# Kernel tuning notes

Hardware: AMD Instinct MI355X
Metric: run time of the kernel (lower is better)

The kernel has to match this reference:

```python
import jax, jax.numpy as jnp
import numpy as np

N, T, D = 2048, 32, 256
NE = T + 2                       # num_embeddings = 32 + 3 - 1
GK_MUL, GK_NUM = 2.0, 3
HEADS = (4, 1)

def _bn(x, g, b):
    # BatchNorm1d (training-mode batch stats, biased variance, eps=1e-5)
    m = x.mean(0)
    v = jnp.mean((x - m) ** 2, 0)
    return (x - m) * jax.lax.rsqrt(v + 1e-5) * g + b

def _gk(x):
    # multi-bandwidth Gaussian kernel over pairwise squared L2 distances
    sq = jnp.sum(x * x, -1)
    l2 = jnp.maximum(sq[:, None] + sq[None, :] - 2.0 * (x @ x.T), 0.0)
    n = x.shape[0]
    bw = jnp.sum(l2) / (n * n - n) / (GK_MUL ** (GK_NUM // 2))
    out = jnp.zeros_like(l2)
    for i in range(GK_NUM):
        out = out + jnp.exp(-l2 / (bw * (GK_MUL ** i)))
    return out

def _mlp3(x, w, b):
    h = jax.nn.relu(x @ w[0] + b[0])
    h = jax.nn.relu(h @ w[1] + b[1])
    return h @ w[2] + b[2]

def _ln(x, g, b):
    m = x.mean(-1, keepdims=True)
    v = jnp.mean((x - m) ** 2, -1, keepdims=True)
    return (x - m) * jax.lax.rsqrt(v + 1e-5) * g + b

def _posenc(t, d):
    pos = jnp.arange(t, dtype=jnp.float32)[:, None]
    div = jnp.exp(jnp.arange(0, d, 2, dtype=jnp.float32) * (-np.log(10000.0) / d))
    ang = pos * div
    return jnp.stack([jnp.sin(ang), jnp.cos(ang)], -1).reshape(t, d)

def _tlayer(x, mask, w, b, w1, b1, w2, b2, g, be, h):
    n, l, d = x.shape
    dh = d // h
    def split(t):
        return t.reshape(n, l, h, dh).transpose(0, 2, 1, 3)
    q = split(x @ w[0] + b[0])
    k = split(x @ w[1] + b[1])
    v = split(x @ w[2] + b[2])
    s = jnp.einsum('bhld,bhmd->bhlm', q, k) / np.sqrt(dh)
    s = jnp.where(mask[:, None, :, :], s, -1e9)
    o = jnp.einsum('bhlm,bhmd->bhld', jax.nn.softmax(s, -1), v)
    o = o.transpose(0, 2, 1, 3).reshape(n, l, d)
    x = _ln(x + o @ w[3] + b[3], g[0], be[0])
    f = jax.nn.relu(x @ w1 + b1) @ w2 + b2
    return _ln(x + f, g[1], be[1])

def _forward(emb0, emb1, emb2, simi_w, simi_b, bn_g, bn_b, simi_eps, dissim,
             gcn_w, gcn_b, adapt_w, adapt_b, type_emb, attn_w, attn_b,
             ffn_w1, ffn_b1, ffn_w2, ffn_b2, ln_g, ln_b,
             out_w1, out_b1, out_w2, out_b2, msk0, msk1, msk2):
    n = emb0.shape[0]
    embs = [emb0[:, 0, :], emb1, emb2]
    msks = [msk0[:, :1], msk1, msk2]               # [n,1] bool each
    mstk = jnp.stack(msks)                         # [3,n,1]
    mask_mats = mstk & jnp.swapaxes(mstk, 1, 2)    # [3,n,n]
    sim_sum = jnp.zeros((n, n), emb0.dtype)
    lstab = jnp.zeros((), emb0.dtype)
    for m in range(3):
        e = embs[m]
        p = _mlp3(e, simi_w[m], simi_b[m])
        wgk = _gk(_bn(jax.nn.relu(p), bn_g, bn_b))
        gk = _gk(_bn(e, bn_g, bn_b))
        eps = jax.nn.sigmoid(simi_eps[m])
        sim_sum = sim_sum + ((1.0 - eps) * wgk + eps) * gk * mask_mats[m]
        lstab = lstab + jnp.abs(jnp.linalg.norm(p) - jnp.linalg.norm(e))
    agg = sim_sum / mask_mats.sum(0).astype(emb0.dtype)
    agg = agg * (agg > jax.nn.sigmoid(dissim[0]))
    imputed = []
    for m in range(3):  # all modals are missing-capable
        h = jax.nn.relu(agg @ (embs[m] @ gcn_w[m, 0]) + gcn_b[m, 0])
        h = jax.nn.relu(agg @ (h @ gcn_w[m, 1]) + gcn_b[m, 1])
        s = jax.nn.sigmoid(embs[m] @ adapt_w[m].T + adapt_b[m])
        o = jax.nn.sigmoid(h @ adapt_w[m].T + adapt_b[m])  # adapt_self reused, bug kept from source
        s = s / (s + o)
        imp = s * embs[m] + (1.0 - s) * h
        mk = msks[m].astype(emb0.dtype)
        imputed.append(imp * mk + (1.0 - mk) * h)
    e0 = emb0.at[:, 0, :].set(imputed[0]) + type_emb[0]
    e0 = e0 + _posenc(emb0.shape[1], emb0.shape[2])
    e1 = imputed[1][:, None, :] + type_emb[1]
    e2 = imputed[2][:, None, :] + type_emb[2]
    z = jnp.concatenate([e0, e1, e2], 1)            # [n, NE, D]
    tok = jnp.concatenate([msk0, msk1, msk2], 1)    # [n, NE]
    amask = tok[:, :, None] & tok[:, None, :]       # [n, NE, NE]
    for li in range(2):
        z = jax.nn.relu(_tlayer(z, amask, attn_w[li], attn_b[li],
                                ffn_w1[li], ffn_b1[li], ffn_w2[li], ffn_b2[li],
                                ln_g[li], ln_b[li], HEADS[li]))
    comb = z.reshape(n, -1)
    y = jax.nn.relu(comb @ out_w1 + out_b1)
    y = (y @ out_w2 + out_b2).squeeze(-1)
    return y, lstab

def setup_inputs():
    key = jax.random.key(0)
    it = iter(jax.random.split(key, 32))
    def nrm(shape, s):
        return jax.random.normal(next(it), shape, jnp.float32) * s
    return {
        'emb0': nrm((N, T, D), 1.0),
        'emb1': nrm((N, D), 1.0),
        'emb2': nrm((N, D), 1.0),
        'msk0': jax.random.randint(next(it), (N, T), 0, 2).astype(bool),
        'msk1': jnp.ones((N, 1), bool),
        'msk2': jax.random.randint(next(it), (N, 1), 0, 2).astype(bool),
        'simi_w': nrm((3, 3, D, D), 0.06), 'simi_b': jnp.zeros((3, 3, D)),
        'bn_g': jnp.ones((D,)), 'bn_b': jnp.zeros((D,)),
        'simi_eps': jnp.ones((4,)), 'dissim': jnp.full((1,), 2.0),
        'gcn_w': nrm((3, 2, D, D), 0.06), 'gcn_b': jnp.zeros((3, 2, D)),
        'adapt_w': nrm((3, 1, D), 0.06), 'adapt_b': jnp.zeros((3, 1)),
        'type_emb': nrm((3, D), 0.02),
        'attn_w': nrm((2, 4, D, D), 0.06), 'attn_b': jnp.zeros((2, 4, D)),
        'ffn_w1': nrm((2, D, 4 * D), 0.06), 'ffn_b1': jnp.zeros((2, 4 * D)),
        'ffn_w2': nrm((2, 4 * D, D), 0.06), 'ffn_b2': jnp.zeros((2, D)),
        'ln_g': jnp.ones((2, 2, D)), 'ln_b': jnp.zeros((2, 2, D)),
        'out_w1': nrm((NE * D, 2 * D), 0.02), 'out_b1': jnp.zeros((2 * D,)),
        'out_w2': nrm((2 * D, 1), 0.02), 'out_b2': jnp.zeros((1,)),
    }

def reference(emb0, emb1, emb2, msk0, msk1, msk2, simi_w, simi_b, bn_g, bn_b,
              simi_eps, dissim, gcn_w, gcn_b, adapt_w, adapt_b, type_emb,
              attn_w, attn_b, ffn_w1, ffn_b1, ffn_w2, ffn_b2, ln_g, ln_b,
              out_w1, out_b1, out_w2, out_b2):
    return _forward(emb0, emb1, emb2, simi_w, simi_b, bn_g, bn_b, simi_eps,
                    dissim, gcn_w, gcn_b, adapt_w, adapt_b, type_emb, attn_w,
                    attn_b, ffn_w1, ffn_b1, ffn_w2, ffn_b2, ln_g, ln_b,
                    out_w1, out_b1, out_w2, out_b2, msk0, msk1, msk2)
```

## Files before the change

### kernel.cpp

```cpp
#include <hip/hip_runtime.h>
#include <hip/hip_bf16.h>


#define NN 2048
#define DD 256
#define LTOK 34

typedef __attribute__((ext_vector_type(8))) short bf16x8;
typedef __attribute__((ext_vector_type(4))) float f32x4;

__device__ __forceinline__ float bf2f(__hip_bfloat16 x) { return __bfloat162float(x); }
__device__ __forceinline__ __hip_bfloat16 f2bf(float x) { return __float2bfloat16(x); }
__device__ __forceinline__ float us2f(ushort u) {
    unsigned x = (unsigned)u << 16;
    float f;
    __builtin_memcpy(&f, &x, 4);
    return f;
}
__device__ __forceinline__ ushort f2us(float x) {
    __hip_bfloat16 h = f2bf(x);
    ushort u;
    __builtin_memcpy(&u, &h, 2);
    return u;
}

__device__ __forceinline__ float block_reduce_sum256(float v, float* red) {
    for (int o = 32; o > 0; o >>= 1) v += __shfl_down(v, o, 64);
    int tid = threadIdx.x;
    if ((tid & 63) == 0) red[tid >> 6] = v;
    __syncthreads();
    float s = red[0] + red[1] + red[2] + red[3];
    __syncthreads();
    return s;
}

__device__ __forceinline__ int xcd_remap(int lin, int nwg) {
    int q = nwg >> 3, r = nwg & 7;
    int xcd = lin & 7, pos = lin >> 3;
    return (xcd < r ? xcd * (q + 1) : r * (q + 1) + (xcd - r) * q) + pos;
}

__device__ __forceinline__ void stage_tile(const ushort* __restrict__ src,
                                           ushort* lds, int grow0, size_t ldk,
                                           int k0, int wv, int l) {
#pragma unroll
    for (int c = 0; c < 4; ++c) {
        int rowbase = wv * 32 + c * 8;
        int row = rowbase + (l >> 3);
        int sx = ((l & 7) ^ (row & 7)) * 8;
        __builtin_amdgcn_global_load_lds(
            (const __attribute__((address_space(1))) void*)(src + (size_t)(grow0 + row) * ldk + k0 + sx),
            (__attribute__((address_space(3))) void*)(lds + rowbase * 64), 16, 0, 0);
    }
}

__device__ __forceinline__ void stage_tile64(const ushort* __restrict__ src,
                                             ushort* lds, int grow0, size_t ldk,
                                             int k0, int wv, int l) {
#pragma unroll
    for (int c = 0; c < 2; ++c) {
        int rowbase = wv * 16 + c * 8;
        int row = rowbase + (l >> 3);
        int sx = ((l & 7) ^ (row & 7)) * 8;
        __builtin_amdgcn_global_load_lds(
            (const __attribute__((address_space(1))) void*)(src + (size_t)(grow0 + row) * ldk + k0 + sx),
            (__attribute__((address_space(3))) void*)(lds + rowbase * 64), 16, 0, 0);
    }
}

#define MFMA_STEP(ACC)                                                          \
    {                                                                           \
        bf16x8 av[4], bv[4];                                                    \
        _Pragma("unroll") for (int f = 0; f < 4; ++f) {                         \
            int ra = wr * 64 + f * 16 + lr;                                     \
            av[f] = *(const bf16x8*)(As + ra * 64 + (((kk * 4 + l16) ^ (ra & 7)) * 8)); \
            int rb = wc * 64 + f * 16 + lr;                                     \
            bv[f] = *(const bf16x8*)(Bs + rb * 64 + (((kk * 4 + l16) ^ (rb & 7)) * 8)); \
        }                                                                       \
        _Pragma("unroll") for (int mf = 0; mf < 4; ++mf)                        \
            _Pragma("unroll") for (int nf = 0; nf < 4; ++nf)                    \
                ACC[mf][nf] = __builtin_amdgcn_mfma_f32_16x16x32_bf16(          \
                    av[mf], bv[nf], ACC[mf][nf], 0, 0, 0);                      \
    }

template <int OUTM, bool BIAS, bool RELU>
__global__ __launch_bounds__(256) void gemm_mfma(
    const ushort* __restrict__ A, const ushort* __restrict__ Bt,
    const float* __restrict__ bias, void* __restrict__ Cout,
    int M, int N, int K, int ldt)
{
    __shared__ __align__(16) ushort As[128 * 64];
    __shared__ __align__(16) ushort Bs[128 * 64];
    const int gx = gridDim.x;
    int lin = xcd_remap(blockIdx.y * gx + blockIdx.x, gx * gridDim.y);
    const int bm = (lin / gx) * 128, bn = (lin % gx) * 128;
    const int tid = threadIdx.x;
    const int l = tid & 63, wv = tid >> 6;
    const int wr = wv >> 1, wc = wv & 1;
    const int l16 = l >> 4, lr = l & 15;
    const int kpz = K / gridDim.z;
    const int kbeg = blockIdx.z * kpz, kend = kbeg + kpz;
    f32x4 zero = {0.f, 0.f, 0.f, 0.f};
    f32x4 acc[4][4];
#pragma unroll
    for (int i = 0; i < 4; ++i)
#pragma unroll
        for (int j = 0; j < 4; ++j) acc[i][j] = zero;

    for (int k0 = kbeg; k0 < kend; k0 += 64) {
        stage_tile(A, As, bm, K, k0, wv, l);
        stage_tile(Bt, Bs, bn, K, k0, wv, l);
        __syncthreads();
#pragma unroll
        for (int kk = 0; kk < 2; ++kk) MFMA_STEP(acc)
        __syncthreads();
    }
    float* Cf = (float*)Cout + (size_t)blockIdx.z * M * N;
#pragma unroll
    for (int mf = 0; mf < 4; ++mf) {
#pragma unroll
        for (int nf = 0; nf < 4; ++nf) {
            int col = bn + wc * 64 + nf * 16 + lr;
            float bb = BIAS ? bias[col] : 0.f;
#pragma unroll
            for (int r = 0; r < 4; ++r) {
                int row = bm + wr * 64 + mf * 16 + l16 * 4 + r;
                float v = acc[mf][nf][r] + bb;
                if (OUTM == 3)
                    v += bf2f(((const __hip_bfloat16*)Cout)[(size_t)row * N + col]);
                if (RELU) v = fmaxf(v, 0.f);
                if (OUTM == 0)
                    Cf[(size_t)row * N + col] = v;
                else if (OUTM == 4) {
                    int r2 = row + 14 * (row / 34);
                    ((__hip_bfloat16*)Cout)[(size_t)col * ldt + r2] = f2bf(v);
                } else
                    ((__hip_bfloat16*)Cout)[(size_t)row * N + col] = f2bf(v);
            }
        }
    }
}

template <int OUTM, bool BIAS, bool RELU>
__global__ __launch_bounds__(256) void gemm_thin(
    const ushort* __restrict__ A, const ushort* __restrict__ Bt,
    const float* __restrict__ bias, void* __restrict__ Cout,
    int M, int N, int K)
{
    __shared__ __align__(16) ushort As[64 * 64];
    __shared__ __align__(16) ushort Bs[128 * 64];
    const int gx = gridDim.x;
    int lin = xcd_remap(blockIdx.y * gx + blockIdx.x, gx * gridDim.y);
    const int bm = (lin / gx) * 64, bn = (lin % gx) * 128;
    const int tid = threadIdx.x;
    const int l = tid & 63, wv = tid >> 6;
    const int wr = wv >> 1, wc = wv & 1;
    const int l16 = l >> 4, lr = l & 15;
    f32x4 zero = {0.f, 0.f, 0.f, 0.f};
    f32x4 acc[2][4];
#pragma unroll
    for (int i = 0; i < 2; ++i)
#pragma unroll
        for (int j = 0; j < 4; ++j) acc[i][j] = zero;

    for (int k0 = 0; k0 < K; k0 += 64) {
        stage_tile64(A, As, bm, K, k0, wv, l);
        stage_tile(Bt, Bs, bn, K, k0, wv, l);
        __syncthreads();
#pragma unroll
        for (int kk = 0; kk < 2; ++kk) {
            bf16x8 av[2], bv[4];
#pragma unroll
            for (int f = 0; f < 2; ++f) {
                int ra = wr * 32 + f * 16 + lr;
                av[f] = *(const bf16x8*)(As + ra * 64 + (((kk * 4 + l16) ^ (ra & 7)) * 8));
            }
#pragma unroll
            for (int f = 0; f < 4; ++f) {
                int rb = wc * 64 + f * 16 + lr;
                bv[f] = *(const bf16x8*)(Bs + rb * 64 + (((kk * 4 + l16) ^ (rb & 7)) * 8));
            }
#pragma unroll
            for (int mf = 0; mf < 2; ++mf)
#pragma unroll
                for (int nf = 0; nf < 4; ++nf)
                    acc[mf][nf] = __builtin_amdgcn_mfma_f32_16x16x32_bf16(
                        av[mf], bv[nf], acc[mf][nf], 0, 0, 0);
        }
        __syncthreads();
    }
#pragma unroll
    for (int mf = 0; mf < 2; ++mf) {
#pragma unroll
        for (int nf = 0; nf < 4; ++nf) {
            int col = bn + wc * 64 + nf * 16 + lr;
            float bb = BIAS ? bias[col] : 0.f;
#pragma unroll
            for (int r = 0; r < 4; ++r) {
                int row = bm + wr * 32 + mf * 16 + l16 * 4 + r;
                float v = acc[mf][nf][r] + bb;
                if (OUTM == 3)
                    v += bf2f(((const __hip_bfloat16*)Cout)[(size_t)row * N + col]);
                if (RELU) v = fmaxf(v, 0.f);
                ((__hip_bfloat16*)Cout)[(size_t)row * N + col] = f2bf(v);
            }
        }
    }
}

template <int OUTM, bool RELU, bool BIAS, bool PSUM>
__global__ __launch_bounds__(256) void gemm_batch(
    const ushort* __restrict__ A, int lda, size_t aoffZ,
    const ushort* __restrict__ Bt, size_t boffZ,
    const float* __restrict__ bias, int biasoffZ,
    void* __restrict__ Cout, int ldc, size_t coffZ,
    float* __restrict__ psum, int M, int N, int K)
{
    __shared__ __align__(16) ushort As[128 * 64];
    __shared__ __align__(16) ushort Bs[128 * 64];
    __shared__ float red[8];
    const int gx = gridDim.x;
    const int lin0 = blockIdx.y * gx + blockIdx.x;
    int lin = xcd_remap(lin0, gx * gridDim.y);
    const int bm = (lin / gx) * 128, bn = (lin % gx) * 128;
    const int z = blockIdx.z;
    A += (size_t)z * aoffZ;
    Bt += (size_t)z * boffZ;
    if (BIAS) bias += (size_t)z * biasoffZ;
    const int tid = threadIdx.x;
    const int l = tid & 63, wv = tid >> 6;
    const int wr = wv >> 1, wc = wv & 1;
    const int l16 = l >> 4, lr = l & 15;
    f32x4 zero = {0.f, 0.f, 0.f, 0.f};
    f32x4 acc[4][4];
#pragma unroll
    for (int i = 0; i < 4; ++i)
#pragma unroll
        for (int j = 0; j < 4; ++j) acc[i][j] = zero;

    for (int k0 = 0; k0 < K; k0 += 64) {
        stage_tile(A, As, bm, lda, k0, wv, l);
        stage_tile(Bt, Bs, bn, K, k0, wv, l);
        __syncthreads();
#pragma unroll
        for (int kk = 0; kk < 2; ++kk) MFMA_STEP(acc)
        __syncthreads();
    }
    float lsq = 0.f;
#pragma unroll
    for (int mf = 0; mf < 4; ++mf) {
#pragma unroll
        for (int nf = 0; nf < 4; ++nf) {
            int col = bn + wc * 64 + nf * 16 + lr;
            float bb = BIAS ? bias[col] : 0.f;
#pragma unroll
            for (int r = 0; r < 4; ++r) {
                int row = bm + wr * 64 + mf * 16 + l16 * 4 + r;
                float v = acc[mf][nf][r] + bb;
                if (RELU) v = fmaxf(v, 0.f);
                if (PSUM) lsq += v * v;
                if (OUTM == 0)
                    ((float*)Cout + (size_t)z * coffZ)[(size_t)row * ldc + col] = v;
                else if (OUTM == 2)
                    ((__hip_bfloat16*)Cout + (size_t)z * coffZ)[(size_t)col * M + row] = f2bf(v);
                else
                    ((__hip_bfloat16*)Cout + (size_t)z * coffZ)[(size_t)row * ldc + col] = f2bf(v);
            }
        }
    }
    if (PSUM) {
        float bs = block_reduce_sum256(lsq, red);
        if (tid == 0) psum[z * gx * gridDim.y + lin0] = bs;
    }
}

__global__ __launch_bounds__(256) void gemm_dist_gk3(
    const ushort* __restrict__ XB6, const float* __restrict__ SQ6,
    const float* __restrict__ bws, const int* __restrict__ MK,
    const float* __restrict__ epsp, ushort* __restrict__ S3b)
{
    __shared__ __align__(16) ushort As[128 * 64];
    __shared__ __align__(16) ushort Bs[128 * 64];
    const int gx = gridDim.x;
    int lin = xcd_remap(blockIdx.y * gx + blockIdx.x, gx * gridDim.y);
    const int bm = (lin / gx) * 128, bn = (lin % gx) * 128;
    const int z = blockIdx.z;
    const ushort* XB = XB6 + (size_t)(2 * z) * NN * DD;
    const float* SQ = SQ6 + (size_t)(2 * z) * NN;
    const int* mk = MK + (size_t)z * NN;
    ushort* S = S3b + (size_t)z * NN * NN;
    const int tid = threadIdx.x;
    const int l = tid & 63, wv = tid >> 6;
    const int wr = wv >> 1, wc = wv & 1;
    const int l16 = l >> 4, lr = l & 15;
    f32x4 zero = {0.f, 0.f, 0.f, 0.f};
    f32x4 acc1[4][4], acc2[4][4];
#pragma unroll
    for (int i = 0; i < 4; ++i)
#pragma unroll
        for (int j = 0; j < 4; ++j) { acc1[i][j] = zero; acc2[i][j] = zero; }

    for (int k0 = 0; k0 < 256; k0 += 64) {
        stage_tile(XB, As, bm, 256, k0, wv, l);
        stage_tile(XB, Bs, bn, 256, k0, wv, l);
        __syncthreads();
#pragma unroll
        for (int kk = 0; kk < 2; ++kk) MFMA_STEP(acc1)
        __syncthreads();
    }
    const ushort* X1 = XB + (size_t)NN * DD;
    for (int k0 = 0; k0 < 256; k0 += 64) {
        stage_tile(X1, As, bm, 256, k0, wv, l);
        stage_tile(X1, Bs, bn, 256, k0, wv, l);
        __syncthreads();
#pragma unroll
        for (int kk = 0; kk < 2; ++kk) MFMA_STEP(acc2)
        __syncthreads();
    }
    float eps = 1.f / (1.f + __expf(-epsp[z]));
    const float cnn = 1.f / ((float)NN * NN - (float)NN);
    float ia4 = 0.5f / (bws[2 * z] * cnn);
    float ib4 = 0.5f / (bws[2 * z + 1] * cnn);
#pragma unroll
    for (int mf = 0; mf < 4; ++mf) {
#pragma unroll
        for (int nf = 0; nf < 4; ++nf) {
            int col = bn + wc * 64 + nf * 16 + lr;
            int mcol = mk[col];
            float sqc0 = SQ[col], sqc1 = SQ[NN + col];
#pragma unroll
            for (int r = 0; r < 4; ++r) {
                int row = bm + wr * 64 + mf * 16 + l16 * 4 + r;
                float d1 = fmaxf(SQ[row] + sqc0 - 2.f * acc1[mf][nf][r], 0.f);
                float d2 = fmaxf(SQ[NN + row] + sqc1 - 2.f * acc2[mf][nf][r], 0.f);
                float t = __expf(-d1 * ia4);
                float t2 = t * t;
                float w = t + t2 + t2 * t2;
                float u = __expf(-d2 * ib4);
                float u2 = u * u;
                float g = u + u2 + u2 * u2;
                float val = ((1.f - eps) * w + eps) * g;
                val = (mk[row] && mcol) ? val : 0.f;
                S[(size_t)row * NN + col] = f2us(val);
            }
        }
    }
}

__global__ __launch_bounds__(256) void bw_fast6(const float* __restrict__ SQ6,
                                                const float* __restrict__ bnb,
                                                float* __restrict__ SCbw) {
    __shared__ float red[8];
    int z = blockIdx.x, tid = threadIdx.x;
    float s1p = 0.f;
    for (int r = tid; r < NN; r += 256) s1p += SQ6[z * NN + r];
    float b = bnb[tid];
    float s1 = block_reduce_sum256(s1p, red);
    float b2 = block_reduce_sum256(b * b, red);
    if (tid == 0)
        SCbw[z] = 2.f * (float)NN * s1 - 2.f * (float)NN * (float)NN * b2;
}

template <int Z, bool RELU>
__global__ __launch_bounds__(256) void slice_fin(const float* __restrict__ SL,
                                                 const float* __restrict__ bias,
                                                 __hip_bfloat16* __restrict__ out,
                                                 int N, size_t MN) {
    size_t v = (size_t)blockIdx.x * 256 + threadIdx.x;
    const float4* S4 = (const float4*)SL;
    size_t MN4 = MN >> 2;
    float4 s = S4[v];
#pragma unroll
    for (int z = 1; z < Z; ++z) {
        float4 t = S4[(size_t)z * MN4 + v];
        s.x += t.x; s.y += t.y; s.z += t.z; s.w += t.w;
    }
    float4 bb = ((const float4*)bias)[v % (size_t)(N >> 2)];
    s.x += bb.x; s.y += bb.y; s.z += bb.z; s.w += bb.w;
    if (RELU) {
        s.x = fmaxf(s.x, 0.f); s.y = fmaxf(s.y, 0.f);
        s.z = fmaxf(s.z, 0.f); s.w = fmaxf(s.w, 0.f);
    }
    union { __hip_bfloat16 h[4]; ushort4 u; } pk;
    pk.h[0] = f2bf(s.x); pk.h[1] = f2bf(s.y);
    pk.h[2] = f2bf(s.z); pk.h[3] = f2bf(s.w);
    ((ushort4*)out)[v] = pk.u;
}

__global__ void cvt_flat(const float* __restrict__ in, __hip_bfloat16* __restrict__ out,
                         int n4) {
    int i = blockIdx.x * 256 + threadIdx.x;
    if (i < n4) {
        float4 v = ((const float4*)in)[i];
        union { __hip_bfloat16 h[4]; ushort4 u; } pk;
        pk.h[0] = f2bf(v.x); pk.h[1] = f2bf(v.y);
        pk.h[2] = f2bf(v.z); pk.h[3] = f2bf(v.w);
        ((ushort4*)out)[i] = pk.u;
    }
}

__global__ __launch_bounds__(256) void cvt_transz(const float* __restrict__ in,
                                                  __hip_bfloat16* __restrict__ out,
                                                  int R, int C) {
    __shared__ float t[32][33];
    size_t zo = (size_t)blockIdx.z * R * C;
    in += zo;
    out += zo;
    int bc = blockIdx.x * 32, br = blockIdx.y * 32;
    int tx = threadIdx.x & 31, ty = threadIdx.x >> 5;
#pragma unroll
    for (int i = 0; i < 32; i += 8)
        t[ty + i][tx] = in[(size_t)(br + ty + i) * C + bc + tx];
    __syncthreads();
#pragma unroll
    for (int i = 0; i < 32; i += 8)
        out[(size_t)(bc + ty + i) * R + br + tx] = f2bf(t[tx][ty + i]);
}

__global__ __launch_bounds__(256) void agg_cvt3(
    const ushort4* __restrict__ S3b, const int* __restrict__ mk0,
    const int* __restrict__ mk1, const int* __restrict__ mk2,
    const float* __restrict__ dissim, ushort4* __restrict__ Sb) {
    size_t v = (size_t)blockIdx.x * 256 + threadIdx.x;
    const size_t PL = (size_t)NN * NN / 4;
    int i = (int)(v >> 9);
    int j0 = (int)((v & 511) << 2);
    float thr = 1.f / (1.f + __expf(-dissim[0]));
    ushort4 u0 = S3b[v], u1 = S3b[PL + v], u2 = S3b[2 * PL + v];
    int m0i = mk0[i], m1i = mk1[i], m2i = mk2[i];
    union { __hip_bfloat16 h[4]; ushort4 u; } pk;
#define AGGC(C0, C1, C2, J)                                                       \
    {                                                                             \
        int j = j0 + J;                                                           \
        int cnt = ((m0i && mk0[j]) ? 1 : 0) + ((m1i && mk1[j]) ? 1 : 0) +         \
                  ((m2i && mk2[j]) ? 1 : 0);                                      \
        float a = cnt ? (us2f(C0) + us2f(C1) + us2f(C2)) / (float)cnt : 0.f;      \
        pk.h[J] = f2bf((a > thr) ? a : 0.f);                                      \
    }
    AGGC(u0.x, u1.x, u2.x, 0) AGGC(u0.y, u1.y, u2.y, 1)
    AGGC(u0.z, u1.z, u2.z, 2) AGGC(u0.w, u1.w, u2.w, 3)
#undef AGGC
    Sb[v] = pk.u;
}

__global__ __launch_bounds__(256) void colstats6(const float* __restrict__ P3,
                                                 const float* __restrict__ E0,
                                                 const float* __restrict__ e1,
                                                 const float* __restrict__ e2,
                                                 float* __restrict__ mv, int nrows) {
    __shared__ float red[8];
    int c = blockIdx.x, z = blockIdx.y, tid = threadIdx.x;
    int m = z >> 1, kind = z & 1;
    const float* X = kind ? (m == 0 ? E0 : (m == 1 ? e1 : e2))
                          : P3 + (size_t)m * NN * DD;
    float s = 0.f, sq = 0.f;
    for (int r = tid; r < nrows; r += 256) {
        float v = X[(size_t)r * DD + c];
        if (!kind) v = fmaxf(v, 0.f);
        s += v; sq += v * v;
    }
    float ts = block_reduce_sum256(s, red);
    float tq = block_reduce_sum256(sq, red);
    if (tid == 0) {
        float mmean = ts / (float)nrows;
        mv[z * 512 + c] = mmean;
        mv[z * 512 + 256 + c] = tq / (float)nrows - mmean * mmean;
    }
}

__global__ __launch_bounds__(256) void bn_fuse6(const float* __restrict__ P3,
                                                const float* __restrict__ E0,
                                                const float* __restrict__ e1,
                                                const float* __restrict__ e2,
                                                const float* __restrict__ mv,
                                                const float* __restrict__ g,
                                                const float* __restrict__ b,
                                                ushort* __restrict__ XB6,
                                                float* __restrict__ SQ6) {
    __shared__ float red[8];
    int r = blockIdx.x, z = blockIdx.y, c = threadIdx.x;
    int m = z >> 1, kind = z & 1;
    const float* X = kind ? (m == 0 ? E0 : (m == 1 ? e1 : e2))
                          : P3 + (size_t)m * NN * DD;
    float v = X[(size_t)r * DD + c];
    if (!kind) v = fmaxf(v, 0.f);
    float y = (v - mv[z * 512 + c]) * rsqrtf(mv[z * 512 + 256 + c] + 1e-5f) * g[c] + b[c];
    __hip_bfloat16 yb = f2bf(y);
    XB6[(size_t)z * NN * DD + (size_t)r * DD + c] = *(ushort*)&yb;
    float yr = bf2f(yb);
    float s = block_reduce_sum256(yr * yr, red);
    if (c == 0) SQ6[z * NN + r] = s;
}

__global__ __launch_bounds__(256) void sumsq_partial(const float* __restrict__ X, int n,
                                                     float* __restrict__ part) {
    __shared__ float red[8];
    int tid = threadIdx.x;
    float s = 0.f;
    for (size_t idx = (size_t)blockIdx.x * 256 + tid; idx < (size_t)n;
         idx += (size_t)gridDim.x * 256) {
        float v = X[idx];
        s += v * v;
    }
    float bs = block_reduce_sum256(s, red);
    if (tid == 0) part[blockIdx.x] = bs;
}

__global__ __launch_bounds__(256) void reduce6(const float* __restrict__ part,
                                               float* __restrict__ SC) {
    __shared__ float red[8];
    int b = blockIdx.x, tid = threadIdx.x;
    const float* src; int n, dst;
    if (b < 3) { src = part + 512 + b * 512; n = 512; dst = 9 + b; }
    else { src = part + 2048 + (b - 3) * 32; n = 32; dst = 6 + (b - 3); }
    float s = 0.f;
    for (int i = tid; i < n; i += 256) s += src[i];
    float bs = block_reduce_sum256(s, red);
    if (tid == 0) SC[dst] = bs;
}

__global__ __launch_bounds__(256) void impute_k(
    const float* __restrict__ E, const __hip_bfloat16* __restrict__ H, int ldh,
    const float* __restrict__ aw, const float* __restrict__ ab,
    const int* __restrict__ mk, float* __restrict__ OUT) {
    __shared__ float red[8];
    int i = blockIdx.x, tid = threadIdx.x;
    float e = E[(size_t)i * DD + tid], h = bf2f(H[(size_t)i * ldh + tid]), w = aw[tid];
    float se = block_reduce_sum256(e * w, red);
    float sh = block_reduce_sum256(h * w, red);
    float s = 1.f / (1.f + __expf(-(se + ab[0])));
    float o = 1.f / (1.f + __expf(-(sh + ab[0])));
    s = s / (s + o);
    float imp = s * e + (1.f - s) * h;
    float m = mk[i] ? 1.f : 0.f;
    OUT[(size_t)i * DD + tid] = imp * m + (1.f - m) * h;
}

__global__ void detect_mode(const void* __restrict__ m1, int* __restrict__ modep) {
    if (threadIdx.x == 0 && blockIdx.x == 0) {
        int vi = ((const int*)m1)[0];
        float vf = ((const float*)m1)[0];
        modep[0] = (vi == 1) ? 0 : ((vf == 1.0f) ? 2 : 1);
    }
}

__device__ __forceinline__ int rd_mask(const void* p, int idx, int mode) {
    if (mode == 0) return ((const int*)p)[idx] != 0;
    if (mode == 1) return ((const unsigned char*)p)[idx] != 0;
    return ((const float*)p)[idx] != 0.f;
}

__global__ void build_masks(const void* __restrict__ m0, const void* __restrict__ m1,
                            const void* __restrict__ m2, const int* __restrict__ modep,
                            int* __restrict__ MK, int* __restrict__ TOK) {
    int mode = modep[0];
    int idx = blockIdx.x * 256 + threadIdx.x;
    if (idx < NN) {
        MK[idx] = rd_mask(m0, idx * 32, mode);
        MK[NN + idx] = rd_mask(m1, idx, mode);
        MK[2 * NN + idx] = rd_mask(m2, idx, mode);
    }
    if (idx < NN * LTOK) {
        int i = idx / LTOK, t = idx - i * LTOK;
        TOK[idx] = (t < 32) ? rd_mask(m0, i * 32 + t, mode)
                            : ((t == 32) ? rd_mask(m1, i, mode) : rd_mask(m2, i, mode));
    }
}

__global__ void gather_e0(const float* __restrict__ emb0, float* __restrict__ E0,
                          __hip_bfloat16* __restrict__ E0b) {
    int i = blockIdx.x, c = threadIdx.x;
    float v = emb0[(size_t)i * 32 * DD + c];
    E0[(size_t)i * DD + c] = v;
    E0b[(size_t)i * DD + c] = f2bf(v);
}

__global__ void pe_table(const float* __restrict__ type_emb, float* __restrict__ PET) {
    int t = blockIdx.x, c = threadIdx.x;
    float div = __expf((float)((c >> 1) << 1) * (-9.210340371976184f / 256.f));
    float ang = (float)t * div;
    float pe = (c & 1) ? __cosf(ang) : __sinf(ang);
    PET[t * 256 + c] = type_emb[c] + pe;
}

__global__ void build_z2(const float4* __restrict__ emb0, const float4* __restrict__ i0,
                         const float4* __restrict__ i1, const float4* __restrict__ i2,
                         const float4* __restrict__ PET,
                         const float4* __restrict__ type_emb,
                         ushort4* __restrict__ Z) {
    int idx = blockIdx.x * 256 + threadIdx.x;
    int c4 = idx & 63;
    int t = (idx >> 6) % LTOK;
    int i = idx / (LTOK * 64);
    float4 v, a;
    if (t < 32) {
        v = (t == 0) ? i0[(size_t)i * 64 + c4]
                     : emb0[((size_t)i * 32 + t) * 64 + c4];
        a = PET[t * 64 + c4];
    } else if (t == 32) {
        v = i1[(size_t)i * 64 + c4];
        a = type_emb[64 + c4];
    } else {
        v = i2[(size_t)i * 64 + c4];
        a = type_emb[128 + c4];
    }
    union { __hip_bfloat16 h[4]; ushort4 u; } pk;
    pk.h[0] = f2bf(v.x + a.x); pk.h[1] = f2bf(v.y + a.y);
    pk.h[2] = f2bf(v.z + a.z); pk.h[3] = f2bf(v.w + a.w);
    Z[idx] = pk.u;
}

template <int DH, int NH>
__global__ __launch_bounds__(256) void attn_mfma(
    const ushort* __restrict__ QKb, const ushort* __restrict__ VTb,
    const int* __restrict__ tok, __hip_bfloat16* __restrict__ O,
    int sample0, int vtld)
{
    __shared__ float S_lds[48][49];
    __shared__ ushort P_lds[48][72];
    __shared__ int tok_lds[34];
    const int s = blockIdx.x;
    const int tid = threadIdx.x;
    const int wv = tid >> 6, l = tid & 63, lr = l & 15, l16 = l >> 4;
    const int rowQ = s * 34;
    if (tid < 34) tok_lds[tid] = tok[(size_t)(sample0 + s) * LTOK + tid];
    const float scale = rsqrtf((float)DH);
    __syncthreads();
#pragma unroll
    for (int h = 0; h < NH; ++h) {
        for (int t = wv; t < 9; t += 4) {
            int mj = t / 3, ni = t % 3;
            f32x4 acc = {0.f, 0.f, 0.f, 0.f};
#pragma unroll
            for (int ks = 0; ks < DH / 32; ++ks) {
                bf16x8 a = *(const bf16x8*)(QKb +
                    (size_t)(rowQ + mj * 16 + lr) * 512 + 256 + h * DH + ks * 32 + l16 * 8);
                bf16x8 b = *(const bf16x8*)(QKb +
                    (size_t)(rowQ + ni * 16 + lr) * 512 + h * DH + ks * 32 + l16 * 8);
                acc = __builtin_amdgcn_mfma_f32_16x16x32_bf16(a, b, acc, 0, 0, 0);
            }
#pragma unroll
            for (int r = 0; r < 4; ++r)
                S_lds[mj * 16 + l16 * 4 + r][ni * 16 + lr] = acc[r];
        }
        __syncthreads();
        if (tid < 48) {
            int i = tid;
            if (i < 34) {
                int ti = tok_lds[i];
                float sc[34];
                float mx = -1e30f;
#pragma unroll
                for (int j = 0; j < 34; ++j) {
                    float v = (ti && tok_lds[j]) ? S_lds[j][i] * scale : -1e9f;
                    sc[j] = v;
                    mx = fmaxf(mx, v);
                }
                float sum = 0.f;
#pragma unroll
                for (int j = 0; j < 34; ++j) {
                    sc[j] = __expf(sc[j] - mx);
                    sum += sc[j];
                }
                float inv = 1.f / sum;
#pragma unroll
                for (int j = 0; j < 34; ++j) P_lds[i][j] = f2us(sc[j] * inv);
#pragma unroll
                for (int j = 34; j < 64; ++j) P_lds[i][j] = 0;
            } else {
#pragma unroll
                for (int j = 0; j < 64; ++j) P_lds[i][j] = 0;
            }
        }
        __syncthreads();
        for (int nt = wv; nt < DH / 16; nt += 4) {
            f32x4 acc[3];
#pragma unroll
            for (int mi = 0; mi < 3; ++mi) acc[mi] = (f32x4){0.f, 0.f, 0.f, 0.f};
#pragma unroll
            for (int ks = 0; ks < 2; ++ks) {
                int j0 = ks * 32 + l16 * 8;
                bf16x8 bv = {0, 0, 0, 0, 0, 0, 0, 0};
                if (j0 < 40) {
                    bv = *(const bf16x8*)(VTb +
                        (size_t)(h * DH + nt * 16 + lr) * vtld + s * 48 + j0);
                    if (j0 == 32) {
                        bv[2] = 0; bv[3] = 0; bv[4] = 0;
                        bv[5] = 0; bv[6] = 0; bv[7] = 0;
                    }
                }
#pragma unroll
                for (int mi = 0; mi < 3; ++mi) {
                    bf16x8 av = *(const bf16x8*)(&P_lds[0][0] + (mi * 16 + lr) * 72 + j0);
                    acc[mi] = __builtin_amdgcn_mfma_f32_16x16x32_bf16(av, bv, acc[mi], 0, 0, 0);
                }
            }
#pragma unroll
            for (int mi = 0; mi < 3; ++mi)
#pragma unroll
                for (int r = 0; r < 4; ++r) {
                    int i = mi * 16 + l16 * 4 + r;
                    if (i < 34)
                        O[(size_t)(rowQ + i) * 256 + h * DH + nt * 16 + lr] =
                            f2bf(acc[mi][r]);
                }
        }
        __syncthreads();
    }
}

template <bool RELU>
__global__ __launch_bounds__(256) void ln_rows(__hip_bfloat16* __restrict__ Z,
                                               const float* __restrict__ g,
                                               const float* __restrict__ b) {
    int row = (blockIdx.x << 2) + (threadIdx.x >> 6);
    int l = threadIdx.x & 63;
    ushort4 u = ((ushort4*)(Z + (size_t)row * DD))[l];
    float x0 = us2f(u.x), x1 = us2f(u.y), x2 = us2f(u.z), x3 = us2f(u.w);
    float s = x0 + x1 + x2 + x3;
    for (int o = 1; o < 64; o <<= 1) s += __shfl_xor(s, o, 64);
    float mean = s * (1.f / 256.f);
    float d0 = x0 - mean, d1 = x1 - mean, d2 = x2 - mean, d3 = x3 - mean;
    float q = d0 * d0 + d1 * d1 + d2 * d2 + d3 * d3;
    for (int o = 1; o < 64; o <<= 1) q += __shfl_xor(q, o, 64);
    float rst = rsqrtf(q * (1.f / 256.f) + 1e-5f);
    float4 gg = ((const float4*)g)[l], bb = ((const float4*)b)[l];
    float y0 = d0 * rst * gg.x + bb.x, y1 = d1 * rst * gg.y + bb.y;
    float y2 = d2 * rst * gg.z + bb.z, y3 = d3 * rst * gg.w + bb.w;
    if (RELU) {
        y0 = fmaxf(y0, 0.f); y1 = fmaxf(y1, 0.f);
        y2 = fmaxf(y2, 0.f); y3 = fmaxf(y3, 0.f);
    }
    union { __hip_bfloat16 h[4]; ushort4 v; } pk;
    pk.h[0] = f2bf(y0); pk.h[1] = f2bf(y1); pk.h[2] = f2bf(y2); pk.h[3] = f2bf(y3);
    ((ushort4*)(Z + (size_t)row * DD))[l] = pk.v;
}

__global__ __launch_bounds__(256) void head2(const __hip_bfloat16* __restrict__ Y1,
                                             const float* __restrict__ w,
                                             const float* __restrict__ b,
                                             float* __restrict__ out) {
    __shared__ float red[8];
    int i = blockIdx.x, tid = threadIdx.x;
    float s = bf2f(Y1[(size_t)i * 512 + tid]) * w[tid] +
              bf2f(Y1[(size_t)i * 512 + 256 + tid]) * w[256 + tid];
    float bs = block_reduce_sum256(s, red);
    if (tid == 0) out[i] = bs + b[0];
}

__global__ void lstab_k(const float* __restrict__ SC, float* __restrict__ dst) {
    if (threadIdx.x == 0 && blockIdx.x == 0) {
        float s = 0.f;
        for (int m = 0; m < 3; ++m)
            s += fabsf(sqrtf(SC[6 + m]) - sqrtf(SC[9 + m]));
        dst[0] = s;
    }
}

__global__ void gcn_bias_cat(const float* __restrict__ gcn_b, float* __restrict__ Bcat) {
    int m = blockIdx.x, l = blockIdx.y, c = threadIdx.x;
    Bcat[l * 768 + m * 256 + c] = gcn_b[(m * 2 + l) * 256 + c];
}

#define GEMM(OUTM_, BIAS_, RELU_, A_, Bt_, BI_, C_, M_, N_, K_)                 \
    gemm_mfma<OUTM_, BIAS_, RELU_>                                              \
        <<<dim3((N_) / 128, (M_) / 128), 256, 0, stream>>>(                     \
            (const ushort*)(A_), (const ushort*)(Bt_), (BI_), (void*)(C_),      \
            (M_), (N_), (K_), 0)
#define GEMMZ(A_, Bt_, C_, M_, N_, K_, Z_)                                      \
    gemm_mfma<0, false, false>                                                  \
        <<<dim3((N_) / 128, (M_) / 128, (Z_)), 256, 0, stream>>>(               \
            (const ushort*)(A_), (const ushort*)(Bt_), (const float*)nullptr,   \
            (void*)(C_), (M_), (N_), (K_), 0)
#define GEMMT(OUTM_, BIAS_, RELU_, A_, Bt_, BI_, C_, M_, N_, K_)                \
    gemm_thin<OUTM_, BIAS_, RELU_>                                              \
        <<<dim3((N_) / 128, (M_) / 64), 256, 0, stream>>>(                      \
            (const ushort*)(A_), (const ushort*)(Bt_), (BI_), (void*)(C_),      \
            (M_), (N_), (K_))

extern "C" void kernel_launch(void* const* d_in, const int* in_sizes, int n_in,
                              void* d_out, int out_size, void* d_ws, size_t ws_size,
                              hipStream_t stream) {
    (void)in_sizes; (void)n_in; (void)out_size; (void)ws_size;
    const float* emb0 = (const float*)d_in[0];
    const float* emb1 = (const float*)d_in[1];
    const float* emb2 = (const float*)d_in[2];
    const void* msk0 = d_in[3];
    const void* msk1 = d_in[4];
    const void* msk2 = d_in[5];
    const float* simi_w = (const float*)d_in[6];
    const float* simi_b = (const float*)d_in[7];
    const float* bn_g = (const float*)d_in[8];
    const float* bn_b = (const float*)d_in[9];
    const float* simi_eps = (const float*)d_in[10];
    const float* dissim = (const float*)d_in[11];
    const float* gcn_w = (const float*)d_in[12];
    const float* gcn_b = (const float*)d_in[13];
    const float* adapt_w = (const float*)d_in[14];
    const float* adapt_b = (const float*)d_in[15];
    const float* type_emb = (const float*)d_in[16];
    const float* attn_w = (const float*)d_in[17];
    const float* attn_b = (const float*)d_in[18];
    const float* ffn_w1 = (const float*)d_in[19];
    const float* ffn_b1 = (const float*)d_in[20];
    const float* ffn_w2 = (const float*)d_in[21];
    const float* ffn_b2 = (const float*)d_in[22];
    const float* ln_g = (const float*)d_in[23];
    const float* ln_b = (const float*)d_in[24];
    const float* out_w1 = (const float*)d_in[25];
    const float* out_b1 = (const float*)d_in[26];
    const float* out_w2 = (const float*)d_in[27];
    const float* out_b2 = (const float*)d_in[28];
    float* out = (float*)d_out;

    const int ACH = 1024, ACROWS = ACH * LTOK;
    const int VTLD = ACH * 48;

    char* wp = (char*)d_ws;
    auto alloc = [&](size_t bytes) -> char* {
        char* p = wp;
        wp += (bytes + 255) & ~(size_t)255;
        return p;
    };
    __hip_bfloat16* Zb = (__hip_bfloat16*)alloc((size_t)NN * LTOK * DD * 2);
    char* UN = alloc((size_t)80 * 1024 * 1024);
    ushort* S3b = (ushort*)UN;
    __hip_bfloat16* QKb = (__hip_bfloat16*)UN;
    __hip_bfloat16* VTb = (__hip_bfloat16*)(UN + (size_t)ACROWS * 512 * 2);
    __hip_bfloat16* Ob = (__hip_bfloat16*)(UN + (size_t)ACROWS * 512 * 2 +
                                           (size_t)256 * VTLD * 2);
    __hip_bfloat16* Hfb = (__hip_bfloat16*)UN;
    float* SLICE = (float*)UN;
    __hip_bfloat16* Sb = (__hip_bfloat16*)alloc((size_t)NN * NN * 2);
    float* P3 = (float*)alloc((size_t)3 * NN * DD * 4);
    float* E0 = (float*)alloc((size_t)NN * DD * 4);
    __hip_bfloat16* Eb3 = (__hip_bfloat16*)alloc((size_t)3 * NN * DD * 2);
    __hip_bfloat16* T1b3 = (__hip_bfloat16*)alloc((size_t)3 * NN * DD * 2);
    __hip_bfloat16* T2b3 = (__hip_bfloat16*)alloc((size_t)3 * NN * DD * 2);
    ushort* XB6 = (ushort*)alloc((size_t)6 * NN * DD * 2);
    __hip_bfloat16* TBt3 = (__hip_bfloat16*)alloc((size_t)3 * NN * DD * 2);
    __hip_bfloat16* HB3 = (__hip_bfloat16*)alloc((size_t)NN * 768 * 2);
    __hip_bfloat16* HB2_3 = (__hip_bfloat16*)alloc((size_t)NN * 768 * 2);
    float* I0 = (float*)alloc((size_t)NN * DD * 4);
    float* I1 = (float*)alloc((size_t)NN * DD * 4);
    float* I2 = (float*)alloc((size_t)NN * DD * 4);
    __hip_bfloat16* Y1b = (__hip_bfloat16*)alloc((size_t)NN * 512 * 2);
    __hip_bfloat16* simi_wt = (__hip_bfloat16*)alloc((size_t)9 * 65536 * 2);
    __hip_bfloat16* gcn_wt = (__hip_bfloat16*)alloc((size_t)6 * 65536 * 2);
    __hip_bfloat16* attn_wt = (__hip_bfloat16*)alloc((size_t)8 * 65536 * 2);
    __hip_bfloat16* w1t = (__hip_bfloat16*)alloc((size_t)2 * 262144 * 2);
    __hip_bfloat16* w2t = (__hip_bfloat16*)alloc((size_t)2 * 262144 * 2);
    __hip_bfloat16* ow1t = (__hip_bfloat16*)alloc((size_t)8704 * 512 * 2);
    float* PET = (float*)alloc(32 * 256 * 4);
    float* MV6 = (float*)alloc(6 * 512 * 4);
    float* SQ6 = (float*)alloc(6 * NN * 4);
    float* PART = (float*)alloc(4096 * 4);
    float* SC = (float*)alloc(64 * 4);
    float* Bcat = (float*)alloc(1536 * 4);
    int* TOK = (int*)alloc((size_t)NN * LTOK * 4);
    int* MK = (int*)alloc((size_t)3 * NN * 4);

    cvt_transz<<<dim3(8, 8, 9), 256, 0, stream>>>(simi_w, simi_wt, 256, 256);
    cvt_transz<<<dim3(8, 8, 6), 256, 0, stream>>>(gcn_w, gcn_wt, 256, 256);
    cvt_transz<<<dim3(8, 8, 8), 256, 0, stream>>>(attn_w, attn_wt, 256, 256);
    cvt_transz<<<dim3(32, 8, 2), 256, 0, stream>>>(ffn_w1, w1t, 256, 1024);
    cvt_transz<<<dim3(8, 32, 2), 256, 0, stream>>>(ffn_w2, w2t, 1024, 256);
    cvt_transz<<<dim3(16, 272, 1), 256, 0, stream>>>(out_w1, ow1t, 8704, 512);

    pe_table<<<32, 256, 0, stream>>>(type_emb, PET);
    gather_e0<<<NN, 256, 0, stream>>>(emb0, E0, Eb3);
    cvt_flat<<<512, 256, 0, stream>>>(emb1, Eb3 + (size_t)NN * DD, NN * DD / 4);
    cvt_flat<<<512, 256, 0, stream>>>(emb2, Eb3 + (size_t)2 * NN * DD, NN * DD / 4);
    detect_mode<<<1, 64, 0, stream>>>(msk1, (int*)SC + 16);
    build_masks<<<(NN * LTOK + 255) / 256, 256, 0, stream>>>(msk0, msk1, msk2,
                                                             (int*)SC + 16, MK, TOK);
    gcn_bias_cat<<<dim3(3, 2), 256, 0, stream>>>(gcn_b, Bcat);

    const float* Ef[3] = {E0, emb1, emb2};

    for (int m = 0; m < 3; ++m)
        sumsq_partial<<<512, 256, 0, stream>>>(Ef[m], NN * DD, PART + 512 + m * 512);
    gemm_batch<1, true, true, false><<<dim3(2, 16, 3), 256, 0, stream>>>(
        (const ushort*)Eb3, 256, (size_t)NN * DD, (const ushort*)simi_wt,
        (size_t)3 * 65536, simi_b, 3 * 256, T1b3, 256, (size_t)NN * DD,
        nullptr, NN, 256, 256);
    gemm_batch<1, true, true, false><<<dim3(2, 16, 3), 256, 0, stream>>>(
        (const ushort*)T1b3, 256, (size_t)NN * DD, (const ushort*)(simi_wt + 65536),
        (size_t)3 * 65536, simi_b + 256, 3 * 256, T2b3, 256, (size_t)NN * DD,
        nullptr, NN, 256, 256);
    gemm_batch<0, false, true, true><<<dim3(2, 16, 3), 256, 0, stream>>>(
        (const ushort*)T2b3, 256, (size_t)NN * DD, (const ushort*)(simi_wt + 2 * 65536),
        (size_t)3 * 65536, simi_b + 2 * 256, 3 * 256, P3, 256, (size_t)NN * DD,
        PART + 2048, NN, 256, 256);
    reduce6<<<6, 256, 0, stream>>>(PART, SC);

    colstats6<<<dim3(256, 6), 256, 0, stream>>>(P3, E0, emb1, emb2, MV6, NN);
    bn_fuse6<<<dim3(NN, 6), 256, 0, stream>>>(P3, E0, emb1, emb2, MV6, bn_g, bn_b,
                                              XB6, SQ6);
    bw_fast6<<<6, 256, 0, stream>>>(SQ6, bn_b, SC + 20);

    gemm_dist_gk3<<<dim3(16, 16, 3), 256, 0, stream>>>(XB6, SQ6, SC + 20, MK,
                                                       simi_eps, S3b);

    agg_cvt3<<<4096, 256, 0, stream>>>((const ushort4*)S3b, MK, MK + NN, MK + 2 * NN,
                                       dissim, (ushort4*)Sb);
    gemm_batch<2, false, false, false><<<dim3(2, 16, 3), 256, 0, stream>>>(
        (const ushort*)Eb3, 256, (size_t)NN * DD, (const ushort*)gcn_wt,
        (size_t)2 * 65536, nullptr, 0, TBt3, 256, (size_t)NN * DD,
        nullptr, NN, 256, 256);
    GEMMZ(Sb, TBt3, SLICE, NN, 768, NN, 8);
    slice_fin<8, true><<<1536, 256, 0, stream>>>(SLICE, Bcat, HB3, 768,
                                                 (size_t)NN * 768);
    gemm_batch<2, false, false, false><<<dim3(2, 16, 3), 256, 0, stream>>>(
        (const ushort*)HB3, 768, (size_t)256, (const ushort*)(gcn_wt + 65536),
        (size_t)2 * 65536, nullptr, 0, TBt3, 256, (size_t)NN * DD,
        nullptr, NN, 256, 256);
    GEMMZ(Sb, TBt3, SLICE, NN, 768, NN, 8);
    slice_fin<8, true><<<1536, 256, 0, stream>>>(SLICE, Bcat + 768, HB2_3, 768,
                                                 (size_t)NN * 768);
    float* IMP[3] = {I0, I1, I2};
    for (int m = 0; m < 3; ++m)
        impute_k<<<NN, 256, 0, stream>>>(Ef[m], HB2_3 + m * 256, 768,
                                         adapt_w + m * 256, adapt_b + m,
                                         MK + m * NN, IMP[m]);

    build_z2<<<NN * LTOK * 64 / 256, 256, 0, stream>>>(
        (const float4*)emb0, (const float4*)I0, (const float4*)I1, (const float4*)I2,
        (const float4*)PET, (const float4*)type_emb, (ushort4*)Zb);
    const int NCHUNK = NN / ACH;
    for (int li = 0; li < 2; ++li) {
        for (int c = 0; c < NCHUNK; ++c) {
            __hip_bfloat16* Zc = Zb + (size_t)c * ACROWS * DD;
            GEMM(1, true, false, Zc, attn_wt + (size_t)(li * 4) * 65536,
                 attn_b + li * 4 * 256, QKb, ACROWS, 512, 256);
            gemm_mfma<4, true, false><<<dim3(2, ACROWS / 128), 256, 0, stream>>>(
                (const ushort*)Zc, (const ushort*)(attn_wt + (size_t)(li * 4 + 2) * 65536),
                attn_b + (li * 4 + 2) * 256, (void*)VTb, ACROWS, 256, 256, VTLD);
            if (li == 0)
                attn_mfma<64, 4><<<ACH, 256, 0, stream>>>(
                    (const ushort*)QKb, (const ushort*)VTb, TOK, Ob, c * ACH, VTLD);
            else
                attn_mfma<256, 1><<<ACH, 256, 0, stream>>>(
                    (const ushort*)QKb, (const ushort*)VTb, TOK, Ob, c * ACH, VTLD);
            GEMMT(3, true, false, Ob, attn_wt + (size_t)(li * 4 + 3) * 65536,
                  attn_b + (li * 4 + 3) * 256, Zc, ACROWS, 256, 256);
        }
        ln_rows<false><<<NN * LTOK / 4, 256, 0, stream>>>(Zb, ln_g + (li * 2 + 0) * 256,
                                                          ln_b + (li * 2 + 0) * 256);
        for (int c = 0; c < NCHUNK; ++c) {
            __hip_bfloat16* Zc = Zb + (size_t)c * ACROWS * DD;
            GEMM(1, true, true, Zc, w1t + (size_t)li * 262144, ffn_b1 + li * 1024,
                 Hfb, ACROWS, 1024, 256);
            GEMMT(3, true, false, Hfb, w2t + (size_t)li * 262144, ffn_b2 + li * 256,
                  Zc, ACROWS, 256, 1024);
        }
        ln_rows<true><<<NN * LTOK / 4, 256, 0, stream>>>(Zb, ln_g + (li * 2 + 1) * 256,
                                                         ln_b + (li * 2 + 1) * 256);
    }

    GEMMZ(Zb, ow1t, SLICE, NN, 512, LTOK * DD, 8);
    slice_fin<8, true><<<1024, 256, 0, stream>>>(SLICE, out_b1, Y1b, 512,
                                                 (size_t)NN * 512);
    head2<<<NN, 256, 0, stream>>>(Y1b, out_w2, out_b2, out);
    lstab_k<<<1, 64, 0, stream>>>(SC, out + NN);
}
```

Baseline: 1.036 ms.

## Store split-K partials in bf16 and fuse QK and V projection GEMMs

The split-K GEMMs now write their partial sums as bf16 instead of fp32, and the reduction kernel reads bf16, which halves the traffic for the partial buffers. The Q/K projection and the transposed V projection are merged into one GEMM launch with N=768, using a new output mode that sends the first 512 columns row-major and the rest into the transposed V layout. The risk is precision loss from rounding each of the eight partial sums to bf16 before they are added. The merge also assumes the V buffer sits directly after QKb at M*512 elements, so it relies on the workspace layout.

```diff
diff --git a/kernel.cpp b/kernel.cpp
--- a/kernel.cpp
+++ b/kernel.cpp
@@ -116,6 +116,7 @@
         __syncthreads();
     }
     float* Cf = (float*)Cout + (size_t)blockIdx.z * M * N;
+    __hip_bfloat16* Cb = (__hip_bfloat16*)Cout + (size_t)blockIdx.z * M * N;
 #pragma unroll
     for (int mf = 0; mf < 4; ++mf) {
 #pragma unroll
@@ -131,9 +132,19 @@
                 if (RELU) v = fmaxf(v, 0.f);
                 if (OUTM == 0)
                     Cf[(size_t)row * N + col] = v;
+                else if (OUTM == 5)
+                    Cb[(size_t)row * N + col] = f2bf(v);
                 else if (OUTM == 4) {
                     int r2 = row + 14 * (row / 34);
                     ((__hip_bfloat16*)Cout)[(size_t)col * ldt + r2] = f2bf(v);
+                } else if (OUTM == 6) {
+                    if (col < 512) {
+                        ((__hip_bfloat16*)Cout)[(size_t)row * 512 + col] = f2bf(v);
+                    } else {
+                        int r2 = row + 14 * (row / 34);
+                        ((__hip_bfloat16*)Cout)[(size_t)M * 512 +
+                            (size_t)(col - 512) * ldt + r2] = f2bf(v);
+                    }
                 } else
                     ((__hip_bfloat16*)Cout)[(size_t)row * N + col] = f2bf(v);
             }
@@ -362,28 +373,27 @@
 }
 
 template <int Z, bool RELU>
-__global__ __launch_bounds__(256) void slice_fin(const float* __restrict__ SL,
-                                                 const float* __restrict__ bias,
-                                                 __hip_bfloat16* __restrict__ out,
-                                                 int N, size_t MN) {
+__global__ __launch_bounds__(256) void slice_fin_b(const ushort4* __restrict__ SL,
+                                                   const float* __restrict__ bias,
+                                                   __hip_bfloat16* __restrict__ out,
+                                                   int N, size_t MN) {
     size_t v = (size_t)blockIdx.x * 256 + threadIdx.x;
-    const float4* S4 = (const float4*)SL;
     size_t MN4 = MN >> 2;
-    float4 s = S4[v];
-#pragma unroll
-    for (int z = 1; z < Z; ++z) {
-        float4 t = S4[(size_t)z * MN4 + v];
-        s.x += t.x; s.y += t.y; s.z += t.z; s.w += t.w;
+    float sx = 0.f, sy = 0.f, sz = 0.f, sw = 0.f;
+#pragma unroll
+    for (int z = 0; z < Z; ++z) {
+        ushort4 t = SL[(size_t)z * MN4 + v];
+        sx += us2f(t.x); sy += us2f(t.y); sz += us2f(t.z); sw += us2f(t.w);
     }
     float4 bb = ((const float4*)bias)[v % (size_t)(N >> 2)];
-    s.x += bb.x; s.y += bb.y; s.z += bb.z; s.w += bb.w;
+    sx += bb.x; sy += bb.y; sz += bb.z; sw += bb.w;
     if (RELU) {
-        s.x = fmaxf(s.x, 0.f); s.y = fmaxf(s.y, 0.f);
-        s.z = fmaxf(s.z, 0.f); s.w = fmaxf(s.w, 0.f);
+        sx = fmaxf(sx, 0.f); sy = fmaxf(sy, 0.f);
+        sz = fmaxf(sz, 0.f); sw = fmaxf(sw, 0.f);
     }
     union { __hip_bfloat16 h[4]; ushort4 u; } pk;
-    pk.h[0] = f2bf(s.x); pk.h[1] = f2bf(s.y);
-    pk.h[2] = f2bf(s.z); pk.h[3] = f2bf(s.w);
+    pk.h[0] = f2bf(sx); pk.h[1] = f2bf(sy);
+    pk.h[2] = f2bf(sz); pk.h[3] = f2bf(sw);
     ((ushort4*)out)[v] = pk.u;
 }
 
@@ -768,7 +778,7 @@
             (const ushort*)(A_), (const ushort*)(Bt_), (BI_), (void*)(C_),      \
             (M_), (N_), (K_), 0)
 #define GEMMZ(A_, Bt_, C_, M_, N_, K_, Z_)                                      \
-    gemm_mfma<0, false, false>                                                  \
+    gemm_mfma<5, false, false>                                                  \
         <<<dim3((N_) / 128, (M_) / 128, (Z_)), 256, 0, stream>>>(               \
             (const ushort*)(A_), (const ushort*)(Bt_), (const float*)nullptr,   \
             (void*)(C_), (M_), (N_), (K_), 0)
@@ -830,7 +840,7 @@
     __hip_bfloat16* Ob = (__hip_bfloat16*)(UN + (size_t)ACROWS * 512 * 2 +
                                            (size_t)256 * VTLD * 2);
     __hip_bfloat16* Hfb = (__hip_bfloat16*)UN;
-    float* SLICE = (float*)UN;
+    __hip_bfloat16* SLICEB = (__hip_bfloat16*)UN;
     __hip_bfloat16* Sb = (__hip_bfloat16*)alloc((size_t)NN * NN * 2);
     float* P3 = (float*)alloc((size_t)3 * NN * DD * 4);
     float* E0 = (float*)alloc((size_t)NN * DD * 4);
@@ -908,16 +918,16 @@
         (const ushort*)Eb3, 256, (size_t)NN * DD, (const ushort*)gcn_wt,
         (size_t)2 * 65536, nullptr, 0, TBt3, 256, (size_t)NN * DD,
         nullptr, NN, 256, 256);
-    GEMMZ(Sb, TBt3, SLICE, NN, 768, NN, 8);
-    slice_fin<8, true><<<1536, 256, 0, stream>>>(SLICE, Bcat, HB3, 768,
-                                                 (size_t)NN * 768);
+    GEMMZ(Sb, TBt3, SLICEB, NN, 768, NN, 8);
+    slice_fin_b<8, true><<<1536, 256, 0, stream>>>((const ushort4*)SLICEB, Bcat, HB3,
+                                                   768, (size_t)NN * 768);
     gemm_batch<2, false, false, false><<<dim3(2, 16, 3), 256, 0, stream>>>(
         (const ushort*)HB3, 768, (size_t)256, (const ushort*)(gcn_wt + 65536),
         (size_t)2 * 65536, nullptr, 0, TBt3, 256, (size_t)NN * DD,
         nullptr, NN, 256, 256);
-    GEMMZ(Sb, TBt3, SLICE, NN, 768, NN, 8);
-    slice_fin<8, true><<<1536, 256, 0, stream>>>(SLICE, Bcat + 768, HB2_3, 768,
-                                                 (size_t)NN * 768);
+    GEMMZ(Sb, TBt3, SLICEB, NN, 768, NN, 8);
+    slice_fin_b<8, true><<<1536, 256, 0, stream>>>((const ushort4*)SLICEB, Bcat + 768,
+                                                   HB2_3, 768, (size_t)NN * 768);
     float* IMP[3] = {I0, I1, I2};
     for (int m = 0; m < 3; ++m)
         impute_k<<<NN, 256, 0, stream>>>(Ef[m], HB2_3 + m * 256, 768,
@@ -931,11 +941,9 @@
     for (int li = 0; li < 2; ++li) {
         for (int c = 0; c < NCHUNK; ++c) {
             __hip_bfloat16* Zc = Zb + (size_t)c * ACROWS * DD;
-            GEMM(1, true, false, Zc, attn_wt + (size_t)(li * 4) * 65536,
-                 attn_b + li * 4 * 256, QKb, ACROWS, 512, 256);
-            gemm_mfma<4, true, false><<<dim3(2, ACROWS / 128), 256, 0, stream>>>(
-                (const ushort*)Zc, (const ushort*)(attn_wt + (size_t)(li * 4 + 2) * 65536),
-                attn_b + (li * 4 + 2) * 256, (void*)VTb, ACROWS, 256, 256, VTLD);
+            gemm_mfma<6, true, false><<<dim3(6, ACROWS / 128), 256, 0, stream>>>(
+                (const ushort*)Zc, (const ushort*)(attn_wt + (size_t)(li * 4) * 65536),
+                attn_b + li * 4 * 256, (void*)QKb, ACROWS, 768, 256, VTLD);
             if (li == 0)
                 attn_mfma<64, 4><<<ACH, 256, 0, stream>>>(
                     (const ushort*)QKb, (const ushort*)VTb, TOK, Ob, c * ACH, VTLD);
@@ -958,9 +966,9 @@
                                                          ln_b + (li * 2 + 1) * 256);
     }
 
-    GEMMZ(Zb, ow1t, SLICE, NN, 512, LTOK * DD, 8);
-    slice_fin<8, true><<<1024, 256, 0, stream>>>(SLICE, out_b1, Y1b, 512,
-                                                 (size_t)NN * 512);
+    GEMMZ(Zb, ow1t, SLICEB, NN, 512, LTOK * DD, 8);
+    slice_fin_b<8, true><<<1024, 256, 0, stream>>>((const ushort4*)SLICEB, out_b1, Y1b,
+                                                   512, (size_t)NN * 512);
     head2<<<NN, 256, 0, stream>>>(Y1b, out_w2, out_b2, out);
     lstab_k<<<1, 64, 0, stream>>>(SC, out + NN);
 }
```

Result: faster. 997.3 us (-3.7%).
